# Kernel tuning notes

Measured on AMD Instinct MI355X. Metric: run time of the kernel, lower is better.

The kernel has to match this reference:

```python
import jax, jax.numpy as jnp
from jax import lax
import numpy as np

FEAT_STRIDE = 16
N_PRE_NMS = 6000
N_POST_NMS = 300
NMS_THRESH = 0.7
MIN_SIZE = 16.0
HH, WW = 100, 152  # feature map size
IN_C, MID_C, N_ANCHOR = 512, 512, 9


def _anchor_base(base=16.0, ratios=(0.5, 1.0, 2.0), scales=(8, 16, 32)):
    py, px = base / 2.0, base / 2.0
    ab = np.zeros((len(ratios) * len(scales), 4), np.float32)
    for i, r in enumerate(ratios):
        for j, s in enumerate(scales):
            h = base * s * np.sqrt(r)
            w = base * s * np.sqrt(1.0 / r)
            ab[i * len(scales) + j] = [py - h / 2, px - w / 2, py + h / 2, px + w / 2]
    return ab


def _shifted_anchors(hh, ww, stride=FEAT_STRIDE):
    ab = _anchor_base()
    sy = np.arange(hh, dtype=np.float32) * stride
    sx = np.arange(ww, dtype=np.float32) * stride
    sx, sy = np.meshgrid(sx, sy)
    shift = np.stack((sy.ravel(), sx.ravel(), sy.ravel(), sx.ravel()), axis=1)
    # [K,A,4] -> [K*A,4]: location-major, anchor-minor (matches loc reshape order)
    return (shift[:, None, :] + ab[None, :, :]).reshape(-1, 4).astype(np.float32)


def _conv2d(x, w, b, pad):
    y = lax.conv_general_dilated(x, w, (1, 1), [(pad, pad), (pad, pad)],
                                 dimension_numbers=("NCHW", "OIHW", "NCHW"))
    return y + b[None, :, None, None]


def _loc2bbox(anchor, loc):
    h = anchor[:, 2] - anchor[:, 0]
    w = anchor[:, 3] - anchor[:, 1]
    cy = anchor[:, 0] + 0.5 * h
    cx = anchor[:, 1] + 0.5 * w
    dy, dx, dh, dw = loc[:, 0], loc[:, 1], loc[:, 2], loc[:, 3]
    cy2 = dy * h + cy
    cx2 = dx * w + cx
    h2 = jnp.exp(dh) * h
    w2 = jnp.exp(dw) * w
    return jnp.stack([cy2 - 0.5 * h2, cx2 - 0.5 * w2, cy2 + 0.5 * h2, cx2 + 0.5 * w2], axis=1)


def _nms_keep(boxes, thresh):
    # boxes sorted by score desc; sequential greedy NMS via fori_loop over a
    # precomputed [N,N] IoU matrix.
    N = boxes.shape[0]
    y1, x1, y2, x2 = boxes[:, 0], boxes[:, 1], boxes[:, 2], boxes[:, 3]
    area = (y2 - y1) * (x2 - x1)
    ih = jnp.clip(jnp.minimum(y2[:, None], y2[None, :]) - jnp.maximum(y1[:, None], y1[None, :]), 0.0)
    iw = jnp.clip(jnp.minimum(x2[:, None], x2[None, :]) - jnp.maximum(x1[:, None], x1[None, :]), 0.0)
    inter = ih * iw
    iou = inter / (area[:, None] + area[None, :] - inter + 1e-9)
    idx = jnp.arange(N)

    def body(i, keep):
        sup = keep[i] & (iou[i] > thresh) & (idx > i)
        return keep & ~sup

    return lax.fori_loop(0, N, body, jnp.ones((N,), bool))


def setup_inputs() -> dict:
    key = jax.random.key(0)
    ks = jax.random.split(key, 4)
    return {
        "x": jax.random.normal(ks[0], (1, IN_C, HH, WW), jnp.float32),
        "conv1_w": 0.01 * jax.random.normal(ks[1], (MID_C, IN_C, 3, 3), jnp.float32),
        "conv1_b": jnp.zeros((MID_C,), jnp.float32),
        "score_w": 0.01 * jax.random.normal(ks[2], (N_ANCHOR * 2, MID_C, 1, 1), jnp.float32),
        "score_b": jnp.zeros((N_ANCHOR * 2,), jnp.float32),
        "loc_w": 0.01 * jax.random.normal(ks[3], (N_ANCHOR * 4, MID_C, 1, 1), jnp.float32),
        "loc_b": jnp.zeros((N_ANCHOR * 4,), jnp.float32),
        "img_h": 1600,
        "img_w": 2432,
    }


def reference(x, conv1_w, conv1_b, score_w, score_b, loc_w, loc_b, img_h, img_w):
    n, _, hh, ww = x.shape
    anchors = jnp.asarray(_shifted_anchors(hh, ww))  # [hh*ww*A, 4]

    h = jax.nn.relu(_conv2d(x, conv1_w, conv1_b, 1))
    rpn_loc = _conv2d(h, loc_w, loc_b, 0).transpose(0, 2, 3, 1).reshape(n, -1, 4)
    scores_hw = _conv2d(h, score_w, score_b, 0).transpose(0, 2, 3, 1)  # [n,hh,ww,2A]
    fg = jax.nn.softmax(scores_hw.reshape(n, hh, ww, N_ANCHOR, 2), axis=-1)[..., 1].reshape(n, -1)
    rpn_score = scores_hw.reshape(n, -1, 2)

    # ProposalCreator (single image)
    roi = _loc2bbox(anchors, rpn_loc[0])
    roi = jnp.stack([
        jnp.clip(roi[:, 0], 0.0, img_h), jnp.clip(roi[:, 1], 0.0, img_w),
        jnp.clip(roi[:, 2], 0.0, img_h), jnp.clip(roi[:, 3], 0.0, img_w)], axis=1)
    valid = ((roi[:, 2] - roi[:, 0]) >= MIN_SIZE) & ((roi[:, 3] - roi[:, 1]) >= MIN_SIZE)
    sc = jnp.where(valid, fg[0], -jnp.inf)

    top_sc, order = lax.top_k(sc, N_PRE_NMS)
    roi_s = roi[order]  # sorted by score desc
    keep = _nms_keep(lax.stop_gradient(roi_s), NMS_THRESH) & (top_sc > -jnp.inf)
    sel_sc, sel = lax.top_k(jnp.where(keep, top_sc, -jnp.inf), N_POST_NMS)
    rois = jnp.where((sel_sc > -jnp.inf)[:, None], roi_s[sel], 0.0)  # [N_POST_NMS,4], zero-padded
    return rpn_loc, rpn_score, rois
```

## Files before the change

### kernel.cpp

```cpp
#include <hip/hip_runtime.h>
#include <math.h>
#include <stdint.h>

#define CHH 100
#define CWW 152
#define NPIX 15200
#define NANCH 136800
#define NPRE 6000
#define NPOST 300
#define CANDCAP 8192
#define MROW 96

#define PSTRIDE 154
#define PPVALID 16016
#define PPS 16128
#define XGUARD 256
#define XROWS_TOTAL (PPS + 2*XGUARD)

#define LPAD 32

#define WTH_OFF  0ull
#define WTL_OFF  4718592ull
#define WX_OFF   9437184ull
#define XH_OFF   9547776ull
#define XL_OFF   26587136ull
#define H_OFF    43626496ull
#define ROI_OFF  76656640ull
#define SC_OFF   78845440ull
#define CTL_OFF  79392640ull
#define CAND_OFF 79396736ull
#define SBOX_OFF 79462272ull

typedef _Float16 f16x8 __attribute__((ext_vector_type(8)));
typedef float    f32x4 __attribute__((ext_vector_type(4)));

struct Ctl {
  unsigned hist[256];
  unsigned prefix;
  unsigned countGreater;
  unsigned candCount;
  unsigned done;
};

struct AnchorArg { float v[36]; };

__device__ __forceinline__ unsigned mono_key(float f) {
  unsigned u = __float_as_uint(f);
  return u ^ ((u & 0x80000000u) ? 0xFFFFFFFFu : 0x80000000u);
}

__device__ __forceinline__ void async_copy16(void* lds, const void* g) {
  __builtin_amdgcn_global_load_lds(
      (const __attribute__((address_space(1))) unsigned int*)g,
      (__attribute__((address_space(3))) unsigned int*)lds,
      16, 0, 0);
}

__global__ __launch_bounds__(256) void prep_w_kernel(const float* __restrict__ w1,
                                                     _Float16* __restrict__ wtapH,
                                                     _Float16* __restrict__ wtapL,
                                                     const float* __restrict__ score_w,
                                                     const float* __restrict__ loc_w,
                                                     float* __restrict__ wx,
                                                     Ctl* __restrict__ ctl) {
  __shared__ float wl[4608];
  const int oc = blockIdx.x, tid = threadIdx.x;
  if (oc == 0) {
    ctl->hist[tid] = 0u;
    if (tid == 0) { ctl->prefix = 0u; ctl->countGreater = 0u; ctl->candCount = 0u; ctl->done = 0u; }
  }
  if (tid < 54) wx[oc * 54 + tid] = (tid < 18) ? score_w[tid * 512 + oc] : loc_w[(tid - 18) * 512 + oc];
  for (int li = tid; li < 4608; li += 256) wl[li] = w1[(size_t)oc * 4608 + li];
  __syncthreads();
  for (int t = 0; t < 9; ++t) {
    size_t ob = ((size_t)t * 512 + oc) * 512;
    for (int ic = tid; ic < 512; ic += 256) {
      float v = wl[ic * 9 + t];
      _Float16 hi = (_Float16)v;
      wtapH[ob + ic] = hi;
      wtapL[ob + ic] = (_Float16)(v - (float)hi);
    }
  }
}

__global__ __launch_bounds__(256) void prep_x_kernel(const float* __restrict__ x,
                                                     _Float16* __restrict__ xh,
                                                     _Float16* __restrict__ xl) {
  __shared__ float tile[64][65];
  const int tid = threadIdx.x;
  const int r0 = blockIdx.x * 64;
  for (int ic0 = 0; ic0 < 512; ic0 += 64) {
    #pragma unroll
    for (int it = 0; it < 16; ++it) {
      int li = it * 256 + tid;
      int i = li >> 6, j = li & 63;
      int pp = r0 + j - XGUARD;
      float v = 0.f;
      if (pp >= 0 && pp < PPVALID) {
        int rowp = pp / PSTRIDE, colp = pp - rowp * PSTRIDE;
        if (rowp >= 1 && rowp <= 100 && colp >= 1 && colp <= 152) {
          int p = (rowp - 1) * CWW + (colp - 1);
          v = x[(size_t)(ic0 + i) * NPIX + p];
        }
      }
      tile[i][j] = v;
    }
    __syncthreads();
    int j = tid >> 2, cq = tid & 3;
    size_t ob = (size_t)(r0 + j) * 512 + ic0 + cq * 16;
    f16x8 vh0, vh1, vl0, vl1;
    #pragma unroll
    for (int c = 0; c < 8; ++c) {
      float v = tile[cq * 16 + c][j];
      _Float16 hi = (_Float16)v;
      vh0[c] = hi; vl0[c] = (_Float16)(v - (float)hi);
    }
    #pragma unroll
    for (int c = 0; c < 8; ++c) {
      float v = tile[cq * 16 + 8 + c][j];
      _Float16 hi = (_Float16)v;
      vh1[c] = hi; vl1[c] = (_Float16)(v - (float)hi);
    }
    *(f16x8*)&xh[ob]     = vh0;
    *(f16x8*)&xh[ob + 8] = vh1;
    *(f16x8*)&xl[ob]     = vl0;
    *(f16x8*)&xl[ob + 8] = vl1;
    __syncthreads();
  }
}

__global__ __launch_bounds__(256) void conv1_mfma_kernel(const _Float16* __restrict__ xh,
                                                         const _Float16* __restrict__ xl,
                                                         const _Float16* __restrict__ wtapH,
                                                         const _Float16* __restrict__ wtapL,
                                                         const float* __restrict__ bias,
                                                         float* __restrict__ h) {
  __shared__ _Float16 Ah[2][128][LPAD], Al[2][128][LPAD], Bh[2][128][LPAD], Bl[2][128][LPAD];
  __shared__ float bsm[128];
  const int tid = threadIdx.x;
  const int bid = blockIdx.x;
  const int oc0 = (bid & 3) * 128;
  const int pp0 = (((bid >> 3) << 1) + ((bid >> 2) & 1)) * 128;
  if (tid < 128) bsm[tid] = bias[oc0 + tid];

  const int lane = tid & 63;
  const int n16 = lane & 15, quad = lane >> 4;
  const int wid = tid >> 6;
  const int wm = wid >> 1, wn = wid & 1;
  const int srow = tid >> 2, sq = tid & 3;
  const int wrow = wid << 4;
  const int sqs  = sq ^ ((srow >> 1) & 3);
  const int cswz = (n16 >> 1) & 3;
  const int rdc  = (quad ^ cswz) * 8;

  const size_t thBase = (size_t)srow * 512 + (size_t)sqs * 8;

  f32x4 acc[4][4];
  #pragma unroll
  for (int mi = 0; mi < 4; ++mi)
    #pragma unroll
    for (int ni = 0; ni < 4; ++ni) acc[mi][ni] = (f32x4){0.f, 0.f, 0.f, 0.f};

  auto stageF = [&](int b, int t, int icb, int dsh) {
    const size_t wOff = ((size_t)t * 512 + oc0) * 512 + (size_t)icb;
    const size_t xOff = (size_t)(pp0 + dsh) * 512 + (size_t)icb;
    #pragma unroll
    for (int hf = 0; hf < 2; ++hf) {
      const int lrow = hf * 64 + wrow;
      const size_t tho = thBase + (size_t)(hf * 64) * 512;
      async_copy16(&Ah[b][lrow][0], wtapH + wOff + tho);
      async_copy16(&Al[b][lrow][0], wtapL + wOff + tho);
      async_copy16(&Bh[b][lrow][0], xh + xOff + tho);
      async_copy16(&Bl[b][lrow][0], xl + xOff + tho);
    }
  };

  stageF(0, 0, 0, -PSTRIDE - 1);
  int tS = 1, icbS = 0, dshS = -PSTRIDE;

  for (int ks = 0; ks < 144; ++ks) {
    const int cur = ks & 1;
    if (ks + 1 < 144) {
      stageF(cur ^ 1, tS, icbS, dshS);
      if (++tS == 9) { tS = 0; icbS += 32; dshS = -PSTRIDE - 1; }
      else dshS += (tS == 3 || tS == 6) ? (PSTRIDE - 2) : 1;
      asm volatile("s_waitcnt vmcnt(8)" ::: "memory");
    } else {
      asm volatile("s_waitcnt vmcnt(0)" ::: "memory");
    }
    __builtin_amdgcn_sched_barrier(0);
    __builtin_amdgcn_s_barrier();
    __builtin_amdgcn_sched_barrier(0);

    f16x8 af[4], ag[4], bf[4], bg[4];
    #pragma unroll
    for (int mi = 0; mi < 4; ++mi) {
      af[mi] = *(const f16x8*)&Ah[cur][wm * 64 + mi * 16 + n16][rdc];
      ag[mi] = *(const f16x8*)&Al[cur][wm * 64 + mi * 16 + n16][rdc];
    }
    #pragma unroll
    for (int ni = 0; ni < 4; ++ni) {
      bf[ni] = *(const f16x8*)&Bh[cur][wn * 64 + ni * 16 + n16][rdc];
      bg[ni] = *(const f16x8*)&Bl[cur][wn * 64 + ni * 16 + n16][rdc];
    }
    asm volatile("s_waitcnt lgkmcnt(0)" ::: "memory");
    __builtin_amdgcn_sched_barrier(0);
    __builtin_amdgcn_s_barrier();
    __builtin_amdgcn_sched_barrier(0);

    __builtin_amdgcn_s_setprio(1);
    #pragma unroll
    for (int mi = 0; mi < 4; ++mi)
      #pragma unroll
      for (int ni = 0; ni < 4; ++ni) {
        acc[mi][ni] = __builtin_amdgcn_mfma_f32_16x16x32_f16(af[mi], bf[ni], acc[mi][ni], 0, 0, 0);
        acc[mi][ni] = __builtin_amdgcn_mfma_f32_16x16x32_f16(af[mi], bg[ni], acc[mi][ni], 0, 0, 0);
        acc[mi][ni] = __builtin_amdgcn_mfma_f32_16x16x32_f16(ag[mi], bf[ni], acc[mi][ni], 0, 0, 0);
      }
    __builtin_amdgcn_s_setprio(0);
  }

  #pragma unroll
  for (int mi = 0; mi < 4; ++mi) {
    int ocb = wm * 64 + mi * 16 + quad * 4;
    #pragma unroll
    for (int ni = 0; ni < 4; ++ni) {
      int pp = pp0 + wn * 64 + ni * 16 + n16;
      #pragma unroll
      for (int r = 0; r < 4; ++r) {
        float v = acc[mi][ni][r] + bsm[ocb + r];
        h[(size_t)(oc0 + ocb + r) * PPS + pp] = fmaxf(v, 0.f);
      }
    }
  }
}

__global__ __launch_bounds__(256) void heads_kernel(const float* __restrict__ h,
                                                    const float* __restrict__ wx,
                                                    const float* __restrict__ score_b,
                                                    const float* __restrict__ loc_b,
                                                    float* __restrict__ rpn_loc,
                                                    float* __restrict__ rpn_score,
                                                    float* __restrict__ roi,
                                                    float* __restrict__ sc,
                                                    AnchorArg ab,
                                                    const int* __restrict__ ihp,
                                                    const int* __restrict__ iwp) {
  __shared__ float hs[64][64];
  __shared__ float red[54][64];
  const int tid = threadIdx.x;
  const int p0 = blockIdx.x * 64;
  const int pxl = tid & 63, icq = tid >> 6;
  const int icu = __builtin_amdgcn_readfirstlane(icq);
  int pcol = p0 + pxl;
  bool pok = pcol < NPIX;
  int ppl = 0;
  if (pok) ppl = (pcol / CWW + 1) * PSTRIDE + (pcol % CWW) + 1;

  float acc[54];
  #pragma unroll
  for (int o = 0; o < 54; ++o) acc[o] = 0.f;

  for (int c = 0; c < 8; ++c) {
    int ic0 = c * 64;
    #pragma unroll
    for (int r = 0; r < 16; ++r) {
      int i = r * 4 + icq;
      hs[i][pxl] = pok ? h[(size_t)(ic0 + i) * PPS + ppl] : 0.f;
    }
    __syncthreads();
    #pragma unroll
    for (int k = 0; k < 16; ++k) {
      int icl = icu + k * 4;
      float v = hs[icl][pxl];
      const float* wrow = &wx[(ic0 + icl) * 54];
      #pragma unroll
      for (int o = 0; o < 54; ++o) acc[o] += wrow[o] * v;
    }
    __syncthreads();
  }
  for (int w = 0; w < 4; ++w) {
    if (icq == w) {
      if (w == 0) {
        #pragma unroll
        for (int o = 0; o < 54; ++o) red[o][pxl] = acc[o];
      } else {
        #pragma unroll
        for (int o = 0; o < 54; ++o) red[o][pxl] += acc[o];
      }
    }
    __syncthreads();
  }

  const float fH = (float)(*ihp);
  const float fW = (float)(*iwp);
  for (int it = tid; it < 576; it += 256) {
    #pragma clang fp contract(off)
    int pl = it / 9, a = it - pl * 9;
    int p = p0 + pl;
    if (p >= NPIX) continue;
    float s0 = red[a * 2][pl]     + score_b[a * 2];
    float s1 = red[a * 2 + 1][pl] + score_b[a * 2 + 1];
    float dy = red[18 + a * 4][pl]     + loc_b[a * 4];
    float dx = red[18 + a * 4 + 1][pl] + loc_b[a * 4 + 1];
    float dh = red[18 + a * 4 + 2][pl] + loc_b[a * 4 + 2];
    float dw = red[18 + a * 4 + 3][pl] + loc_b[a * 4 + 3];
    int row = p * 9 + a;
    *(float2*)&rpn_score[row * 2] = make_float2(s0, s1);
    *(float4*)&rpn_loc[(size_t)row * 4] = make_float4(dy, dx, dh, dw);
    int ypix = p / CWW, xpix = p - ypix * CWW;
    float sy = (float)(ypix * 16), sx = (float)(xpix * 16);
    float a0 = sy + ab.v[a * 4 + 0], a1 = sx + ab.v[a * 4 + 1];
    float a2 = sy + ab.v[a * 4 + 2], a3 = sx + ab.v[a * 4 + 3];
    float ha = a2 - a0, wa = a3 - a1;
    float cy = a0 + 0.5f * ha, cx = a1 + 0.5f * wa;
    float cy2 = dy * ha + cy, cx2 = dx * wa + cx;
    float h2 = expf(dh) * ha, w2 = expf(dw) * wa;
    float y1 = cy2 - 0.5f * h2, x1 = cx2 - 0.5f * w2;
    float y2 = cy2 + 0.5f * h2, x2 = cx2 + 0.5f * w2;
    y1 = fminf(fmaxf(y1, 0.f), fH); x1 = fminf(fmaxf(x1, 0.f), fW);
    y2 = fminf(fmaxf(y2, 0.f), fH); x2 = fminf(fmaxf(x2, 0.f), fW);
    *(float4*)&roi[(size_t)row * 4] = make_float4(y1, x1, y2, x2);
    bool valid = (y2 - y1 >= 16.f) && (x2 - x1 >= 16.f);
    float m  = fmaxf(s0, s1);
    float e0 = expf(s0 - m), e1 = expf(s1 - m);
    float fg = e1 / (e0 + e1);
    sc[row] = valid ? fg : -__builtin_inff();
  }
}

#define HGRID 120
__global__ __launch_bounds__(256) void hist_scan_kernel(const float* __restrict__ sc,
                                                        Ctl* __restrict__ ctl, int pass) {
  __shared__ unsigned hloc[256];
  __shared__ unsigned ticket_s;
  int tid = threadIdx.x;
  hloc[tid] = 0u;
  __syncthreads();
  unsigned prefix = ctl->prefix;
  for (int i = blockIdx.x * 256 + tid; i < NANCH; i += HGRID * 256) {
    unsigned m = mono_key(sc[i]);
    bool pred = (pass == 0) || ((m >> (32 - 8 * pass)) == prefix);
    if (pred) atomicAdd(&hloc[(m >> (24 - 8 * pass)) & 255u], 1u);
  }
  __syncthreads();
  if (hloc[tid]) atomicAdd(&ctl->hist[tid], hloc[tid]);
  __threadfence();
  __syncthreads();
  if (tid == 0) ticket_s = atomicAdd(&ctl->done, 1u);
  __syncthreads();
  if (ticket_s != HGRID - 1) return;
  unsigned v = atomicExch(&ctl->hist[tid], 0u);
  hloc[tid] = v;
  __syncthreads();
  for (int d = 1; d < 256; d <<= 1) {
    unsigned t2 = hloc[tid] + ((tid + d < 256) ? hloc[tid + d] : 0u);
    __syncthreads();
    hloc[tid] = t2;
    __syncthreads();
  }
  unsigned G = ctl->countGreater;
  unsigned inclT = hloc[tid];
  unsigned inclN = (tid < 255) ? hloc[tid + 1] : 0u;
  if (G + inclT >= (unsigned)NPRE && G + inclN < (unsigned)NPRE) {
    ctl->prefix = (prefix << 8) | (unsigned)tid;
    ctl->countGreater = G + inclN;
  }
  if (tid == 0) atomicExch(&ctl->done, 0u);
}

__global__ __launch_bounds__(256) void compact_kernel(const float* __restrict__ sc,
                                                      Ctl* __restrict__ ctl,
                                                      unsigned long long* __restrict__ cand) {
  int i = blockIdx.x * 256 + threadIdx.x;
  unsigned prefix = ctl->prefix;
  bool pred = false; unsigned m = 0;
  if (i < NANCH) { m = mono_key(sc[i]); pred = ((m >> 8) >= prefix); }
  unsigned long long mask = __ballot(pred);
  if (mask) {
    int lane = threadIdx.x & 63;
    int leader = __ffsll((long long)mask) - 1;
    unsigned base = 0;
    if (lane == leader) base = atomicAdd(&ctl->candCount, (unsigned)__popcll(mask));
    base = __shfl(base, leader);
    if (pred) {
      unsigned slot = base + (unsigned)__popcll(mask & ((1ull << lane) - 1ull));
      if (slot < CANDCAP)
        cand[slot] = (((unsigned long long)(~m)) << 32) | (unsigned)i;
    }
  }
}

__global__ __launch_bounds__(256) void rank_kernel(const unsigned long long* __restrict__ cand,
                                                   const Ctl* __restrict__ ctl,
                                                   const float* __restrict__ roi,
                                                   float4* __restrict__ sbox) {
  __shared__ unsigned long long kb[2048];
  __shared__ unsigned pc[64][5];
  const int tid = threadIdx.x;
  const int c = tid & 63, q = tid >> 6;
  const int slot = blockIdx.x * 64 + c;
  unsigned nv = ctl->candCount; if (nv > CANDCAP) nv = CANDCAP;
  unsigned long long K = (slot < (int)nv) ? cand[slot] : ~0ull;
  unsigned cnt = 0;
  for (unsigned c0 = 0; c0 < nv; c0 += 2048) {
    for (int i = tid; i < 2048; i += 256) {
      unsigned g = c0 + (unsigned)i;
      kb[i] = (g < nv) ? cand[g] : ~0ull;
    }
    __syncthreads();
    int lim = (int)(nv - c0); if (lim > 2048) lim = 2048;
    int i0 = q * 512, ie = i0 + 512; if (ie > lim) ie = lim;
    for (int i = i0; i < ie; ++i) cnt += (kb[i] < K) ? 1u : 0u;
    __syncthreads();
  }
  pc[c][q] = cnt;
  __syncthreads();
  if (q == 0) {
    unsigned rank = pc[c][0] + pc[c][1] + pc[c][2] + pc[c][3];
    if (slot < (int)nv && rank < NPRE) {
      unsigned idx = (unsigned)(K & 0xFFFFFFFFull);
      sbox[rank] = *(const float4*)&roi[(size_t)idx * 4];
    }
  } else if (q == 1) {
    int nvR = (nv < (unsigned)NPRE) ? (int)nv : NPRE;
    if (slot >= nvR && slot < NPRE) sbox[slot] = make_float4(0.f, 0.f, 0.f, 0.f);
  }
}

__device__ __forceinline__ bool iou_gt(float4 A, float4 B) {
  float areaA = (A.z - A.x) * (A.w - A.y);
  float areaB = (B.z - B.x) * (B.w - B.y);
  float ih = fmaxf(fminf(A.z, B.z) - fmaxf(A.x, B.x), 0.f);
  float iw = fmaxf(fminf(A.w, B.w) - fmaxf(A.y, B.y), 0.f);
  float inter = ih * iw;
  return inter / (areaA + areaB - inter + 1e-9f) > 0.7f;
}

__global__ __launch_bounds__(64) void mask_kernel(const float4* __restrict__ sbox,
                                                  unsigned long long* __restrict__ M) {
  const int ci = blockIdx.x, cj = blockIdx.y;
  if (cj < ci) return;
  __shared__ float4 cb[64];
  const int tid = threadIdx.x;
  const int i = ci * 64 + tid;
  const int jbase = cj * 64;
  const float4 bi = (i < NPRE) ? sbox[i] : make_float4(0.f, 0.f, 0.f, 0.f);
  cb[tid] = (jbase + tid < NPRE) ? sbox[jbase + tid] : make_float4(0.f, 0.f, 0.f, 0.f);
  __syncthreads();
  if (i >= NPRE) return;
  unsigned long long bits = 0ull;
  #pragma unroll 8
  for (int jj = 0; jj < 64; ++jj) {
    int jg = jbase + jj;
    float4 bj = cb[jj];
    if (jg > i && jg < NPRE && iou_gt(bi, bj)) bits |= (1ull << jj);
  }
  M[(size_t)i * MROW + cj] = bits;
}

__global__ __launch_bounds__(64) void resolve_kernel(const unsigned long long* __restrict__ M,
                                                     const Ctl* __restrict__ ctl,
                                                     const float4* __restrict__ sbox,
                                                     float* __restrict__ rois_out) {
  __shared__ unsigned long long remLDS[94];
  __shared__ int keepList[NPOST];
  __shared__ int keepCount;
  const int l = threadIdx.x;
  unsigned cnt = ctl->candCount; if (cnt > (unsigned)NPRE) cnt = NPRE;
  const int nvalid = (int)cnt;

  auto initw = [&](int w) -> unsigned long long {
    int lo = w * 64;
    if (lo + 64 <= nvalid) return 0ull;
    if (lo >= nvalid) return ~0ull;
    return (~0ull) << (nvalid - lo);
  };
  unsigned long long rem0 = initw(l);
  unsigned long long rem1 = (l < 30) ? initw(64 + l) : ~0ull;

  int keepTotal = 0;
  int cstop = 94;
  unsigned long long dw = M[(size_t)l * MROW + 0];

  for (int c = 0; c < 94; ++c) {
    unsigned long long dwN = 0ull;
    if (c + 1 < 94) dwN = M[(size_t)((c + 1) * 64 + l) * MROW + (c + 1)];

    unsigned long long remRep = (c < 64) ? __shfl(rem0, c) : __shfl(rem1, c - 64);

    #pragma unroll
    for (int kk = 0; kk < 64; kk += 16) {
      unsigned long long wv[16];
      #pragma unroll
      for (int t = 0; t < 16; ++t) wv[t] = __shfl(dw, kk + t);
      #pragma unroll
      for (int t = 0; t < 16; ++t) {
        if (!((remRep >> (kk + t)) & 1ull)) remRep |= wv[t];
      }
    }

    if (l == 0) remLDS[c] = remRep;
    if (c < 64) { if (l == c) rem0 = remRep; }
    else        { if (l == c - 64) rem1 = remRep; }
    keepTotal += (int)__popcll(~remRep);

    unsigned long long km = ~remRep;
    const size_t base = (size_t)c * 64;
    while (km) {
      int k0 = __ffsll((long long)km) - 1; km &= km - 1;
      int k1 = k0, k2 = k0, k3 = k0;
      if (km) { k1 = __ffsll((long long)km) - 1; km &= km - 1; }
      if (km) { k2 = __ffsll((long long)km) - 1; km &= km - 1; }
      if (km) { k3 = __ffsll((long long)km) - 1; km &= km - 1; }
      const unsigned long long* p0 = M + (base + k0) * MROW;
      const unsigned long long* p1 = M + (base + k1) * MROW;
      const unsigned long long* p2 = M + (base + k2) * MROW;
      const unsigned long long* p3 = M + (base + k3) * MROW;
      unsigned long long a0 = p0[l], a1 = p1[l], a2 = p2[l], a3 = p3[l];
      rem0 |= a0 | a1 | a2 | a3;
      if (l < 30) {
        unsigned long long b0 = p0[64 + l], b1 = p1[64 + l], b2 = p2[64 + l], b3 = p3[64 + l];
        rem1 |= b0 | b1 | b2 | b3;
      }
    }

    dw = dwN;
    if (keepTotal >= NPOST) { cstop = c + 1; break; }
  }

  __syncthreads();
  if (l == 0) {
    int ck = 0;
    for (int w = 0; w < cstop && ck < NPOST; ++w) {
      unsigned long long kw = ~remLDS[w];
      while (kw && ck < NPOST) {
        int r = __ffsll((long long)kw) - 1; kw &= kw - 1;
        keepList[ck++] = w * 64 + r;
      }
    }
    keepCount = ck;
  }
  __syncthreads();
  for (int s = l; s < NPOST; s += 64) {
    float4 b = make_float4(0.f, 0.f, 0.f, 0.f);
    if (s < keepCount) b = sbox[keepList[s]];
    *(float4*)&rois_out[(size_t)s * 4] = b;
  }
}

extern "C" void kernel_launch(void* const* d_in, const int* in_sizes, int n_in,
                              void* d_out, int out_size, void* d_ws, size_t ws_size,
                              hipStream_t stream) {
  const float* x  = (const float*)d_in[0];
  const float* w1 = (const float*)d_in[1];
  const float* b1 = (const float*)d_in[2];
  const float* sw = (const float*)d_in[3];
  const float* sb = (const float*)d_in[4];
  const float* lw = (const float*)d_in[5];
  const float* lb = (const float*)d_in[6];
  const int* ihp  = (const int*)d_in[7];
  const int* iwp  = (const int*)d_in[8];
  float* out = (float*)d_out;

  char* ws = (char*)d_ws;
  _Float16* wtapH = (_Float16*)(ws + WTH_OFF);
  _Float16* wtapL = (_Float16*)(ws + WTL_OFF);
  float* wx   = (float*)(ws + WX_OFF);
  _Float16* xh_alloc = (_Float16*)(ws + XH_OFF);
  _Float16* xl_alloc = (_Float16*)(ws + XL_OFF);
  _Float16* xh = xh_alloc + (size_t)XGUARD * 512;
  _Float16* xl = xl_alloc + (size_t)XGUARD * 512;
  float* h    = (float*)(ws + H_OFF);
  float* roi  = (float*)(ws + ROI_OFF);
  float* sc   = (float*)(ws + SC_OFF);
  Ctl*   ctl  = (Ctl*)(ws + CTL_OFF);
  unsigned long long* cand = (unsigned long long*)(ws + CAND_OFF);
  float4* sbox = (float4*)(ws + SBOX_OFF);
  unsigned long long* Mmask = (unsigned long long*)(ws + H_OFF);

  AnchorArg ab;
  {
    const double ratios[3] = {0.5, 1.0, 2.0};
    const double scales[3] = {8.0, 16.0, 32.0};
    for (int i = 0; i < 3; ++i)
      for (int j = 0; j < 3; ++j) {
        double hh = 16.0 * scales[j] * sqrt(ratios[i]);
        double wwd = 16.0 * scales[j] * sqrt(1.0 / ratios[i]);
        int a = i * 3 + j;
        ab.v[a * 4 + 0] = (float)(8.0 - hh / 2.0);
        ab.v[a * 4 + 1] = (float)(8.0 - wwd / 2.0);
        ab.v[a * 4 + 2] = (float)(8.0 + hh / 2.0);
        ab.v[a * 4 + 3] = (float)(8.0 + wwd / 2.0);
      }
  }

  float* rpn_loc   = out;
  float* rpn_score = out + 547200;
  float* rois      = out + 820800;

  prep_w_kernel<<<512, 256, 0, stream>>>(w1, wtapH, wtapL, sw, lw, wx, ctl);
  prep_x_kernel<<<XROWS_TOTAL / 64, 256, 0, stream>>>(x, xh_alloc, xl_alloc);
  conv1_mfma_kernel<<<504, 256, 0, stream>>>(xh, xl, wtapH, wtapL, b1, h);
  heads_kernel<<<238, 256, 0, stream>>>(h, wx, sb, lb, rpn_loc, rpn_score, roi, sc, ab, ihp, iwp);
  for (int p = 0; p < 3; ++p)
    hist_scan_kernel<<<HGRID, 256, 0, stream>>>(sc, ctl, p);
  compact_kernel<<<535, 256, 0, stream>>>(sc, ctl, cand);
  rank_kernel<<<CANDCAP / 64, 256, 0, stream>>>(cand, ctl, roi, sbox);
  mask_kernel<<<dim3(94, 94), 64, 0, stream>>>(sbox, Mmask);
  resolve_kernel<<<1, 64, 0, stream>>>(Mmask, ctl, sbox, rois);
}
```

Before: 637.9 us.

## Fuse selection pipeline into one persistent kernel with grid barriers

```diff
diff --git a/kernel.cpp b/kernel.cpp
--- a/kernel.cpp
+++ b/kernel.cpp
@@ -18,6 +18,8 @@
 #define XROWS_TOTAL (PPS + 2*XGUARD)
 
 #define LPAD 32
+
+#define SBLK 120
 
 #define WTH_OFF  0ull
 #define WTL_OFF  4718592ull
@@ -40,6 +42,7 @@
   unsigned countGreater;
   unsigned candCount;
   unsigned done;
+  unsigned bar[8];
 };
 
 struct AnchorArg { float v[36]; };
@@ -56,76 +59,90 @@
       16, 0, 0);
 }
 
-__global__ __launch_bounds__(256) void prep_w_kernel(const float* __restrict__ w1,
-                                                     _Float16* __restrict__ wtapH,
-                                                     _Float16* __restrict__ wtapL,
-                                                     const float* __restrict__ score_w,
-                                                     const float* __restrict__ loc_w,
-                                                     float* __restrict__ wx,
-                                                     Ctl* __restrict__ ctl) {
-  __shared__ float wl[4608];
-  const int oc = blockIdx.x, tid = threadIdx.x;
-  if (oc == 0) {
-    ctl->hist[tid] = 0u;
-    if (tid == 0) { ctl->prefix = 0u; ctl->countGreater = 0u; ctl->candCount = 0u; ctl->done = 0u; }
-  }
-  if (tid < 54) wx[oc * 54 + tid] = (tid < 18) ? score_w[tid * 512 + oc] : loc_w[(tid - 18) * 512 + oc];
-  for (int li = tid; li < 4608; li += 256) wl[li] = w1[(size_t)oc * 4608 + li];
+__device__ __forceinline__ void gridbar(unsigned* bar, unsigned nblk) {
+  __threadfence();
   __syncthreads();
-  for (int t = 0; t < 9; ++t) {
-    size_t ob = ((size_t)t * 512 + oc) * 512;
-    for (int ic = tid; ic < 512; ic += 256) {
-      float v = wl[ic * 9 + t];
-      _Float16 hi = (_Float16)v;
-      wtapH[ob + ic] = hi;
-      wtapL[ob + ic] = (_Float16)(v - (float)hi);
-    }
-  }
-}
-
-__global__ __launch_bounds__(256) void prep_x_kernel(const float* __restrict__ x,
-                                                     _Float16* __restrict__ xh,
-                                                     _Float16* __restrict__ xl) {
-  __shared__ float tile[64][65];
+  if (threadIdx.x == 0) {
+    unsigned t = atomicAdd(bar, 1u);
+    unsigned target = t - (t % nblk) + nblk;
+    while (atomicAdd(bar, 0u) < target) __builtin_amdgcn_s_sleep(8);
+  }
+  __syncthreads();
+  __threadfence();
+}
+
+__global__ __launch_bounds__(256) void prep_kernel(const float* __restrict__ w1,
+                                                   _Float16* __restrict__ wtapH,
+                                                   _Float16* __restrict__ wtapL,
+                                                   const float* __restrict__ score_w,
+                                                   const float* __restrict__ loc_w,
+                                                   float* __restrict__ wx,
+                                                   Ctl* __restrict__ ctl,
+                                                   const float* __restrict__ x,
+                                                   _Float16* __restrict__ xh,
+                                                   _Float16* __restrict__ xl) {
   const int tid = threadIdx.x;
-  const int r0 = blockIdx.x * 64;
-  for (int ic0 = 0; ic0 < 512; ic0 += 64) {
-    #pragma unroll
-    for (int it = 0; it < 16; ++it) {
-      int li = it * 256 + tid;
-      int i = li >> 6, j = li & 63;
-      int pp = r0 + j - XGUARD;
-      float v = 0.f;
-      if (pp >= 0 && pp < PPVALID) {
-        int rowp = pp / PSTRIDE, colp = pp - rowp * PSTRIDE;
-        if (rowp >= 1 && rowp <= 100 && colp >= 1 && colp <= 152) {
-          int p = (rowp - 1) * CWW + (colp - 1);
-          v = x[(size_t)(ic0 + i) * NPIX + p];
+  if (blockIdx.x < 512) {
+    __shared__ float wl[4608];
+    const int oc = blockIdx.x;
+    if (oc == 0) {
+      ctl->hist[tid] = 0u;
+      if (tid == 0) { ctl->prefix = 0u; ctl->countGreater = 0u; ctl->candCount = 0u; ctl->done = 0u; }
+      if (tid < 8) ctl->bar[tid] = 0u;
+    }
+    if (tid < 54) wx[oc * 54 + tid] = (tid < 18) ? score_w[tid * 512 + oc] : loc_w[(tid - 18) * 512 + oc];
+    for (int li = tid; li < 4608; li += 256) wl[li] = w1[(size_t)oc * 4608 + li];
+    __syncthreads();
+    for (int t = 0; t < 9; ++t) {
+      size_t ob = ((size_t)t * 512 + oc) * 512;
+      for (int ic = tid; ic < 512; ic += 256) {
+        float v = wl[ic * 9 + t];
+        _Float16 hi = (_Float16)v;
+        wtapH[ob + ic] = hi;
+        wtapL[ob + ic] = (_Float16)(v - (float)hi);
+      }
+    }
+  } else {
+    __shared__ float tile[64][65];
+    const int r0 = (blockIdx.x - 512) * 64;
+    for (int ic0 = 0; ic0 < 512; ic0 += 64) {
+      #pragma unroll
+      for (int it = 0; it < 16; ++it) {
+        int li = it * 256 + tid;
+        int i = li >> 6, j = li & 63;
+        int pp = r0 + j - XGUARD;
+        float v = 0.f;
+        if (pp >= 0 && pp < PPVALID) {
+          int rowp = pp / PSTRIDE, colp = pp - rowp * PSTRIDE;
+          if (rowp >= 1 && rowp <= 100 && colp >= 1 && colp <= 152) {
+            int p = (rowp - 1) * CWW + (colp - 1);
+            v = x[(size_t)(ic0 + i) * NPIX + p];
+          }
         }
-      }
-      tile[i][j] = v;
-    }
-    __syncthreads();
-    int j = tid >> 2, cq = tid & 3;
-    size_t ob = (size_t)(r0 + j) * 512 + ic0 + cq * 16;
-    f16x8 vh0, vh1, vl0, vl1;
-    #pragma unroll
-    for (int c = 0; c < 8; ++c) {
-      float v = tile[cq * 16 + c][j];
-      _Float16 hi = (_Float16)v;
-      vh0[c] = hi; vl0[c] = (_Float16)(v - (float)hi);
-    }
-    #pragma unroll
-    for (int c = 0; c < 8; ++c) {
-      float v = tile[cq * 16 + 8 + c][j];
-      _Float16 hi = (_Float16)v;
-      vh1[c] = hi; vl1[c] = (_Float16)(v - (float)hi);
-    }
-    *(f16x8*)&xh[ob]     = vh0;
-    *(f16x8*)&xh[ob + 8] = vh1;
-    *(f16x8*)&xl[ob]     = vl0;
-    *(f16x8*)&xl[ob + 8] = vl1;
-    __syncthreads();
+        tile[i][j] = v;
+      }
+      __syncthreads();
+      int j = tid >> 2, cq = tid & 3;
+      size_t ob = (size_t)(r0 + j) * 512 + ic0 + cq * 16;
+      f16x8 vh0, vh1, vl0, vl1;
+      #pragma unroll
+      for (int c = 0; c < 8; ++c) {
+        float v = tile[cq * 16 + c][j];
+        _Float16 hi = (_Float16)v;
+        vh0[c] = hi; vl0[c] = (_Float16)(v - (float)hi);
+      }
+      #pragma unroll
+      for (int c = 0; c < 8; ++c) {
+        float v = tile[cq * 16 + 8 + c][j];
+        _Float16 hi = (_Float16)v;
+        vh1[c] = hi; vl1[c] = (_Float16)(v - (float)hi);
+      }
+      *(f16x8*)&xh[ob]     = vh0;
+      *(f16x8*)&xh[ob + 8] = vh1;
+      *(f16x8*)&xl[ob]     = vl0;
+      *(f16x8*)&xl[ob + 8] = vl1;
+      __syncthreads();
+    }
   }
 }
 
@@ -245,13 +262,16 @@
                                                     float* __restrict__ sc,
                                                     AnchorArg ab,
                                                     const int* __restrict__ ihp,
-                                                    const int* __restrict__ iwp) {
+                                                    const int* __restrict__ iwp,
+                                                    Ctl* __restrict__ ctl) {
   __shared__ float hs[64][64];
   __shared__ float red[54][64];
+  __shared__ unsigned hloc0[256];
   const int tid = threadIdx.x;
   const int p0 = blockIdx.x * 64;
   const int pxl = tid & 63, icq = tid >> 6;
   const int icu = __builtin_amdgcn_readfirstlane(icq);
+  hloc0[tid] = 0u;
   int pcol = p0 + pxl;
   bool pok = pcol < NPIX;
   int ppl = 0;
@@ -325,31 +345,15 @@
     float m  = fmaxf(s0, s1);
     float e0 = expf(s0 - m), e1 = expf(s1 - m);
     float fg = e1 / (e0 + e1);
-    sc[row] = valid ? fg : -__builtin_inff();
-  }
-}
-
-#define HGRID 120
-__global__ __launch_bounds__(256) void hist_scan_kernel(const float* __restrict__ sc,
-                                                        Ctl* __restrict__ ctl, int pass) {
-  __shared__ unsigned hloc[256];
-  __shared__ unsigned ticket_s;
-  int tid = threadIdx.x;
-  hloc[tid] = 0u;
+    float sv = valid ? fg : -__builtin_inff();
+    sc[row] = sv;
+    atomicAdd(&hloc0[mono_key(sv) >> 24], 1u);
+  }
   __syncthreads();
-  unsigned prefix = ctl->prefix;
-  for (int i = blockIdx.x * 256 + tid; i < NANCH; i += HGRID * 256) {
-    unsigned m = mono_key(sc[i]);
-    bool pred = (pass == 0) || ((m >> (32 - 8 * pass)) == prefix);
-    if (pred) atomicAdd(&hloc[(m >> (24 - 8 * pass)) & 255u], 1u);
-  }
-  __syncthreads();
-  if (hloc[tid]) atomicAdd(&ctl->hist[tid], hloc[tid]);
-  __threadfence();
-  __syncthreads();
-  if (tid == 0) ticket_s = atomicAdd(&ctl->done, 1u);
-  __syncthreads();
-  if (ticket_s != HGRID - 1) return;
+  if (hloc0[tid]) atomicAdd(&ctl->hist[tid], hloc0[tid]);
+}
+
+__device__ __forceinline__ void scan_update(Ctl* __restrict__ ctl, unsigned* hloc, int tid) {
   unsigned v = atomicExch(&ctl->hist[tid], 0u);
   hloc[tid] = v;
   __syncthreads();
@@ -359,72 +363,13 @@
     hloc[tid] = t2;
     __syncthreads();
   }
-  unsigned G = ctl->countGreater;
+  unsigned G = atomicAdd(&ctl->countGreater, 0u);
+  unsigned oldp = atomicAdd(&ctl->prefix, 0u);
   unsigned inclT = hloc[tid];
   unsigned inclN = (tid < 255) ? hloc[tid + 1] : 0u;
   if (G + inclT >= (unsigned)NPRE && G + inclN < (unsigned)NPRE) {
-    ctl->prefix = (prefix << 8) | (unsigned)tid;
-    ctl->countGreater = G + inclN;
-  }
-  if (tid == 0) atomicExch(&ctl->done, 0u);
-}
-
-__global__ __launch_bounds__(256) void compact_kernel(const float* __restrict__ sc,
-                                                      Ctl* __restrict__ ctl,
-                                                      unsigned long long* __restrict__ cand) {
-  int i = blockIdx.x * 256 + threadIdx.x;
-  unsigned prefix = ctl->prefix;
-  bool pred = false; unsigned m = 0;
-  if (i < NANCH) { m = mono_key(sc[i]); pred = ((m >> 8) >= prefix); }
-  unsigned long long mask = __ballot(pred);
-  if (mask) {
-    int lane = threadIdx.x & 63;
-    int leader = __ffsll((long long)mask) - 1;
-    unsigned base = 0;
-    if (lane == leader) base = atomicAdd(&ctl->candCount, (unsigned)__popcll(mask));
-    base = __shfl(base, leader);
-    if (pred) {
-      unsigned slot = base + (unsigned)__popcll(mask & ((1ull << lane) - 1ull));
-      if (slot < CANDCAP)
-        cand[slot] = (((unsigned long long)(~m)) << 32) | (unsigned)i;
-    }
-  }
-}
-
-__global__ __launch_bounds__(256) void rank_kernel(const unsigned long long* __restrict__ cand,
-                                                   const Ctl* __restrict__ ctl,
-                                                   const float* __restrict__ roi,
-                                                   float4* __restrict__ sbox) {
-  __shared__ unsigned long long kb[2048];
-  __shared__ unsigned pc[64][5];
-  const int tid = threadIdx.x;
-  const int c = tid & 63, q = tid >> 6;
-  const int slot = blockIdx.x * 64 + c;
-  unsigned nv = ctl->candCount; if (nv > CANDCAP) nv = CANDCAP;
-  unsigned long long K = (slot < (int)nv) ? cand[slot] : ~0ull;
-  unsigned cnt = 0;
-  for (unsigned c0 = 0; c0 < nv; c0 += 2048) {
-    for (int i = tid; i < 2048; i += 256) {
-      unsigned g = c0 + (unsigned)i;
-      kb[i] = (g < nv) ? cand[g] : ~0ull;
-    }
-    __syncthreads();
-    int lim = (int)(nv - c0); if (lim > 2048) lim = 2048;
-    int i0 = q * 512, ie = i0 + 512; if (ie > lim) ie = lim;
-    for (int i = i0; i < ie; ++i) cnt += (kb[i] < K) ? 1u : 0u;
-    __syncthreads();
-  }
-  pc[c][q] = cnt;
-  __syncthreads();
-  if (q == 0) {
-    unsigned rank = pc[c][0] + pc[c][1] + pc[c][2] + pc[c][3];
-    if (slot < (int)nv && rank < NPRE) {
-      unsigned idx = (unsigned)(K & 0xFFFFFFFFull);
-      sbox[rank] = *(const float4*)&roi[(size_t)idx * 4];
-    }
-  } else if (q == 1) {
-    int nvR = (nv < (unsigned)NPRE) ? (int)nv : NPRE;
-    if (slot >= nvR && slot < NPRE) sbox[slot] = make_float4(0.f, 0.f, 0.f, 0.f);
+    atomicExch(&ctl->prefix, (oldp << 8) | (unsigned)tid);
+    atomicExch(&ctl->countGreater, G + inclN);
   }
 }
 
@@ -437,102 +382,207 @@
   return inter / (areaA + areaB - inter + 1e-9f) > 0.7f;
 }
 
-__global__ __launch_bounds__(64) void mask_kernel(const float4* __restrict__ sbox,
-                                                  unsigned long long* __restrict__ M) {
-  const int ci = blockIdx.x, cj = blockIdx.y;
-  if (cj < ci) return;
-  __shared__ float4 cb[64];
-  const int tid = threadIdx.x;
-  const int i = ci * 64 + tid;
-  const int jbase = cj * 64;
-  const float4 bi = (i < NPRE) ? sbox[i] : make_float4(0.f, 0.f, 0.f, 0.f);
-  cb[tid] = (jbase + tid < NPRE) ? sbox[jbase + tid] : make_float4(0.f, 0.f, 0.f, 0.f);
-  __syncthreads();
-  if (i >= NPRE) return;
-  unsigned long long bits = 0ull;
-  #pragma unroll 8
-  for (int jj = 0; jj < 64; ++jj) {
-    int jg = jbase + jj;
-    float4 bj = cb[jj];
-    if (jg > i && jg < NPRE && iou_gt(bi, bj)) bits |= (1ull << jj);
-  }
-  M[(size_t)i * MROW + cj] = bits;
-}
-
-__global__ __launch_bounds__(64) void resolve_kernel(const unsigned long long* __restrict__ M,
-                                                     const Ctl* __restrict__ ctl,
-                                                     const float4* __restrict__ sbox,
+__global__ __launch_bounds__(256) void select_kernel(const float* __restrict__ sc,
+                                                     Ctl* __restrict__ ctl,
+                                                     unsigned long long* __restrict__ cand,
+                                                     const float* __restrict__ roi,
+                                                     float4* __restrict__ sbox,
+                                                     unsigned long long* __restrict__ M,
+                                                     const float4* __restrict__ sboxro,
                                                      float* __restrict__ rois_out) {
+  __shared__ unsigned hloc[256];
+  __shared__ unsigned bc[1];
+  __shared__ unsigned long long kb[2048];
+  __shared__ unsigned pc[64][5];
+  __shared__ float4 cbw[4][64];
   __shared__ unsigned long long remLDS[94];
   __shared__ int keepList[NPOST];
+  const int tid = threadIdx.x;
+  const int bid = blockIdx.x;
+
+  if (bid == 0) scan_update(ctl, hloc, tid);
+  gridbar(&ctl->bar[0], SBLK);
+
+  #pragma unroll
+  for (int pass = 1; pass <= 2; ++pass) {
+    if (tid == 0) bc[0] = atomicAdd(&ctl->prefix, 0u);
+    hloc[tid] = 0u;
+    __syncthreads();
+    const unsigned prefix = bc[0];
+    const int shp = 32 - 8 * pass, shb = 24 - 8 * pass;
+    for (int i = bid * 256 + tid; i < NANCH; i += SBLK * 256) {
+      unsigned m = mono_key(sc[i]);
+      if ((m >> shp) == prefix) atomicAdd(&hloc[(m >> shb) & 255u], 1u);
+    }
+    __syncthreads();
+    if (hloc[tid]) atomicAdd(&ctl->hist[tid], hloc[tid]);
+    gridbar(&ctl->bar[2 * pass - 1], SBLK);
+    if (bid == 0) scan_update(ctl, hloc, tid);
+    gridbar(&ctl->bar[2 * pass], SBLK);
+  }
+
+  {
+    if (tid == 0) bc[0] = atomicAdd(&ctl->prefix, 0u);
+    __syncthreads();
+    const unsigned prefix = bc[0];
+    for (int base = bid * 256; base < NANCH; base += SBLK * 256) {
+      int i = base + tid;
+      bool pred = false; unsigned m = 0;
+      if (i < NANCH) { m = mono_key(sc[i]); pred = ((m >> 8) >= prefix); }
+      unsigned long long mask = __ballot(pred);
+      if (mask) {
+        int lane = tid & 63;
+        int leader = __ffsll((long long)mask) - 1;
+        unsigned cbase = 0;
+        if (lane == leader) cbase = atomicAdd(&ctl->candCount, (unsigned)__popcll(mask));
+        cbase = __shfl(cbase, leader);
+        if (pred) {
+          unsigned slot = cbase + (unsigned)__popcll(mask & ((1ull << lane) - 1ull));
+          if (slot < CANDCAP)
+            cand[slot] = (((unsigned long long)(~m)) << 32) | (unsigned)i;
+        }
+      }
+    }
+  }
+  gridbar(&ctl->bar[5], SBLK);
+
+  {
+    if (tid == 0) bc[0] = atomicAdd(&ctl->candCount, 0u);
+    __syncthreads();
+    unsigned nv = bc[0]; if (nv > CANDCAP) nv = CANDCAP;
+    const int c = tid & 63, q = tid >> 6;
+    for (int tile = bid; tile < CANDCAP / 64; tile += SBLK) {
+      const int slot = tile * 64 + c;
+      unsigned long long K = (slot < (int)nv) ? cand[slot] : ~0ull;
+      unsigned cnt = 0;
+      for (unsigned c0 = 0; c0 < nv; c0 += 2048) {
+        for (int i = tid; i < 2048; i += 256) {
+          unsigned g = c0 + (unsigned)i;
+          kb[i] = (g < nv) ? cand[g] : ~0ull;
+        }
+        __syncthreads();
+        int lim = (int)(nv - c0); if (lim > 2048) lim = 2048;
+        int i0 = q * 512, ie = i0 + 512; if (ie > lim) ie = lim;
+        for (int i = i0; i < ie; ++i) cnt += (kb[i] < K) ? 1u : 0u;
+        __syncthreads();
+      }
+      pc[c][q] = cnt;
+      __syncthreads();
+      if (q == 0) {
+        unsigned rank = pc[c][0] + pc[c][1] + pc[c][2] + pc[c][3];
+        if (slot < (int)nv && rank < NPRE) {
+          unsigned idx = (unsigned)(K & 0xFFFFFFFFull);
+          sbox[rank] = *(const float4*)&roi[(size_t)idx * 4];
+        }
+      } else if (q == 1) {
+        int nvR = (nv < (unsigned)NPRE) ? (int)nv : NPRE;
+        if (slot >= nvR && slot < NPRE) sbox[slot] = make_float4(0.f, 0.f, 0.f, 0.f);
+      }
+      __syncthreads();
+    }
+  }
+  gridbar(&ctl->bar[6], SBLK);
+
+  {
+    const int wv = tid >> 6, ln = tid & 63;
+    for (int pair = bid * 4 + wv; pair < 94 * 94; pair += SBLK * 4) {
+      int ci = pair / 94, cj = pair - ci * 94;
+      if (cj < ci) continue;
+      const int i = ci * 64 + ln;
+      const int jbase = cj * 64;
+      float4 z = make_float4(0.f, 0.f, 0.f, 0.f);
+      float4 bi = (i < NPRE) ? sboxro[i] : z;
+      cbw[wv][ln] = (jbase + ln < NPRE) ? sboxro[jbase + ln] : z;
+      asm volatile("s_waitcnt lgkmcnt(0)" ::: "memory");
+      if (i < NPRE) {
+        unsigned long long bits = 0ull;
+        #pragma unroll 8
+        for (int jj = 0; jj < 64; ++jj) {
+          int jg = jbase + jj;
+          float4 bj = cbw[wv][jj];
+          if (jg > i && jg < NPRE && iou_gt(bi, bj)) bits |= (1ull << jj);
+        }
+        M[(size_t)i * MROW + cj] = bits;
+      }
+    }
+  }
+  gridbar(&ctl->bar[7], SBLK);
+
+  if (bid != 0) return;
+  if (tid == 0) bc[0] = atomicAdd(&ctl->candCount, 0u);
+  __syncthreads();
+  unsigned cnt = bc[0]; if (cnt > (unsigned)NPRE) cnt = NPRE;
+  const int nvalid = (int)cnt;
   __shared__ int keepCount;
-  const int l = threadIdx.x;
-  unsigned cnt = ctl->candCount; if (cnt > (unsigned)NPRE) cnt = NPRE;
-  const int nvalid = (int)cnt;
-
-  auto initw = [&](int w) -> unsigned long long {
-    int lo = w * 64;
-    if (lo + 64 <= nvalid) return 0ull;
-    if (lo >= nvalid) return ~0ull;
-    return (~0ull) << (nvalid - lo);
-  };
-  unsigned long long rem0 = initw(l);
-  unsigned long long rem1 = (l < 30) ? initw(64 + l) : ~0ull;
-
-  int keepTotal = 0;
-  int cstop = 94;
-  unsigned long long dw = M[(size_t)l * MROW + 0];
-
-  for (int c = 0; c < 94; ++c) {
-    unsigned long long dwN = 0ull;
-    if (c + 1 < 94) dwN = M[(size_t)((c + 1) * 64 + l) * MROW + (c + 1)];
-
-    unsigned long long remRep = (c < 64) ? __shfl(rem0, c) : __shfl(rem1, c - 64);
-
-    #pragma unroll
-    for (int kk = 0; kk < 64; kk += 16) {
-      unsigned long long wv[16];
+  __shared__ int cstop_s;
+
+  if (tid < 64) {
+    const int l = tid;
+    auto initw = [&](int w) -> unsigned long long {
+      int lo = w * 64;
+      if (lo + 64 <= nvalid) return 0ull;
+      if (lo >= nvalid) return ~0ull;
+      return (~0ull) << (nvalid - lo);
+    };
+    unsigned long long rem0 = initw(l);
+    unsigned long long rem1 = (l < 30) ? initw(64 + l) : ~0ull;
+
+    int keepTotal = 0;
+    int cstop = 94;
+    unsigned long long dw = M[(size_t)l * MROW + 0];
+
+    for (int c = 0; c < 94; ++c) {
+      unsigned long long dwN = 0ull;
+      if (c + 1 < 94) dwN = M[(size_t)((c + 1) * 64 + l) * MROW + (c + 1)];
+
+      unsigned long long remRep = (c < 64) ? __shfl(rem0, c) : __shfl(rem1, c - 64);
+
       #pragma unroll
-      for (int t = 0; t < 16; ++t) wv[t] = __shfl(dw, kk + t);
-      #pragma unroll
-      for (int t = 0; t < 16; ++t) {
-        if (!((remRep >> (kk + t)) & 1ull)) remRep |= wv[t];
-      }
-    }
-
-    if (l == 0) remLDS[c] = remRep;
-    if (c < 64) { if (l == c) rem0 = remRep; }
-    else        { if (l == c - 64) rem1 = remRep; }
-    keepTotal += (int)__popcll(~remRep);
-
-    unsigned long long km = ~remRep;
-    const size_t base = (size_t)c * 64;
-    while (km) {
-      int k0 = __ffsll((long long)km) - 1; km &= km - 1;
-      int k1 = k0, k2 = k0, k3 = k0;
-      if (km) { k1 = __ffsll((long long)km) - 1; km &= km - 1; }
-      if (km) { k2 = __ffsll((long long)km) - 1; km &= km - 1; }
-      if (km) { k3 = __ffsll((long long)km) - 1; km &= km - 1; }
-      const unsigned long long* p0 = M + (base + k0) * MROW;
-      const unsigned long long* p1 = M + (base + k1) * MROW;
-      const unsigned long long* p2 = M + (base + k2) * MROW;
-      const unsigned long long* p3 = M + (base + k3) * MROW;
-      unsigned long long a0 = p0[l], a1 = p1[l], a2 = p2[l], a3 = p3[l];
-      rem0 |= a0 | a1 | a2 | a3;
-      if (l < 30) {
-        unsigned long long b0 = p0[64 + l], b1 = p1[64 + l], b2 = p2[64 + l], b3 = p3[64 + l];
-        rem1 |= b0 | b1 | b2 | b3;
-      }
-    }
-
-    dw = dwN;
-    if (keepTotal >= NPOST) { cstop = c + 1; break; }
+      for (int kk = 0; kk < 64; kk += 16) {
+        unsigned long long wvv[16];
+        #pragma unroll
+        for (int t = 0; t < 16; ++t) wvv[t] = __shfl(dw, kk + t);
+        #pragma unroll
+        for (int t = 0; t < 16; ++t) {
+          if (!((remRep >> (kk + t)) & 1ull)) remRep |= wvv[t];
+        }
+      }
+
+      if (l == 0) remLDS[c] = remRep;
+      if (c < 64) { if (l == c) rem0 = remRep; }
+      else        { if (l == c - 64) rem1 = remRep; }
+      keepTotal += (int)__popcll(~remRep);
+
+      unsigned long long km = ~remRep;
+      const size_t base = (size_t)c * 64;
+      while (km) {
+        int k0 = __ffsll((long long)km) - 1; km &= km - 1;
+        int k1 = k0, k2 = k0, k3 = k0;
+        if (km) { k1 = __ffsll((long long)km) - 1; km &= km - 1; }
+        if (km) { k2 = __ffsll((long long)km) - 1; km &= km - 1; }
+        if (km) { k3 = __ffsll((long long)km) - 1; km &= km - 1; }
+        const unsigned long long* p0 = M + (base + k0) * MROW;
+        const unsigned long long* p1 = M + (base + k1) * MROW;
+        const unsigned long long* p2 = M + (base + k2) * MROW;
+        const unsigned long long* p3 = M + (base + k3) * MROW;
+        unsigned long long a0 = p0[l], a1 = p1[l], a2 = p2[l], a3 = p3[l];
+        rem0 |= a0 | a1 | a2 | a3;
+        if (l < 30) {
+          unsigned long long b0 = p0[64 + l], b1 = p1[64 + l], b2 = p2[64 + l], b3 = p3[64 + l];
+          rem1 |= b0 | b1 | b2 | b3;
+        }
+      }
+
+      dw = dwN;
+      if (keepTotal >= NPOST) { cstop = c + 1; break; }
+    }
+    if (l == 0) cstop_s = cstop;
   }
 
   __syncthreads();
-  if (l == 0) {
+  if (tid == 0) {
     int ck = 0;
-    for (int w = 0; w < cstop && ck < NPOST; ++w) {
+    for (int w = 0; w < cstop_s && ck < NPOST; ++w) {
       unsigned long long kw = ~remLDS[w];
       while (kw && ck < NPOST) {
         int r = __ffsll((long long)kw) - 1; kw &= kw - 1;
@@ -542,9 +592,9 @@
     keepCount = ck;
   }
   __syncthreads();
-  for (int s = l; s < NPOST; s += 64) {
+  for (int s = tid; s < NPOST; s += 256) {
     float4 b = make_float4(0.f, 0.f, 0.f, 0.f);
-    if (s < keepCount) b = sbox[keepList[s]];
+    if (s < keepCount) b = sboxro[keepList[s]];
     *(float4*)&rois_out[(size_t)s * 4] = b;
   }
 }
@@ -599,14 +649,9 @@
   float* rpn_score = out + 547200;
   float* rois      = out + 820800;
 
-  prep_w_kernel<<<512, 256, 0, stream>>>(w1, wtapH, wtapL, sw, lw, wx, ctl);
-  prep_x_kernel<<<XROWS_TOTAL / 64, 256, 0, stream>>>(x, xh_alloc, xl_alloc);
+  prep_kernel<<<512 + XROWS_TOTAL / 64, 256, 0, stream>>>(w1, wtapH, wtapL, sw, lw, wx, ctl,
+                                                          x, xh_alloc, xl_alloc);
   conv1_mfma_kernel<<<504, 256, 0, stream>>>(xh, xl, wtapH, wtapL, b1, h);
-  heads_kernel<<<238, 256, 0, stream>>>(h, wx, sb, lb, rpn_loc, rpn_score, roi, sc, ab, ihp, iwp);
-  for (int p = 0; p < 3; ++p)
-    hist_scan_kernel<<<HGRID, 256, 0, stream>>>(sc, ctl, p);
-  compact_kernel<<<535, 256, 0, stream>>>(sc, ctl, cand);
-  rank_kernel<<<CANDCAP / 64, 256, 0, stream>>>(cand, ctl, roi, sbox);
-  mask_kernel<<<dim3(94, 94), 64, 0, stream>>>(sbox, Mmask);
-  resolve_kernel<<<1, 64, 0, stream>>>(Mmask, ctl, sbox, rois);
-}
+  heads_kernel<<<238, 256, 0, stream>>>(h, wx, sb, lb, rpn_loc, rpn_score, roi, sc, ab, ihp, iwp, ctl);
+  select_kernel<<<SBLK, 256, 0, stream>>>(sc, ctl, cand, roi, sbox, Mmask, sbox, rois);
+}
```

After: 862.5 us. +35.2%, slower.
